# Kernel tuning notes

Measured on AMD Instinct MI355X. Metric: run time of the kernel, lower is better.

## Reference

```python
import jax, jax.numpy as jnp
import numpy as np

DIM = 64   # model dim == d_inner (expand=1)
Hh = 64
Ww = 64
BATCH = 4
D_IN = 64
N_ST = 8   # d_state
DT_R = 4   # dt_rank = ceil(dim/16)
K = 4      # depthwise conv kernel
NB = 8     # total CrossMambaBlocks: 4 (depth=1) + 4 final cross blocks


def setup_inputs():
    key = jax.random.key(0)
    ks = iter(jax.random.split(key, 40))
    def rn(shape, s=0.02):
        return jax.random.normal(next(ks), shape, jnp.float32) * s
    A_init = jnp.log(jnp.tile(jnp.arange(1, N_ST + 1, dtype=jnp.float32), (NB, D_IN, 1)))
    return dict(
        img1=rn((BATCH, DIM, Hh, Ww), 1.0), img2=rn((BATCH, DIM, Hh, Ww), 1.0),
        img1_sum=rn((BATCH, DIM, Hh, Ww), 1.0), img2_sum=rn((BATCH, DIM, Hh, Ww), 1.0),
        norm0_w=jnp.ones((NB, DIM)), norm0_b=jnp.zeros((NB, DIM)),
        norm1_w=jnp.ones((NB, DIM)), norm1_b=jnp.zeros((NB, DIM)),
        in_w=rn((NB, 2 * D_IN, DIM)), in_b=jnp.zeros((NB, 2 * D_IN)),
        conv_w_f=rn((NB, D_IN, 1, K), 0.1), conv_b_f=jnp.zeros((NB, D_IN)),
        conv_w_b=rn((NB, D_IN, 1, K), 0.1), conv_b_b=jnp.zeros((NB, D_IN)),
        xproj_w_f=rn((NB, DT_R + 2 * N_ST, D_IN)), xproj_w_b=rn((NB, DT_R + 2 * N_ST, D_IN)),
        dtproj_w_f=rn((NB, D_IN, DT_R), 0.1), dtproj_b_f=jnp.zeros((NB, D_IN)),
        dtproj_w_b=rn((NB, D_IN, DT_R), 0.1), dtproj_b_b=jnp.zeros((NB, D_IN)),
        A_log_f=A_init, A_log_b=A_init,
        D_f=jnp.ones((NB, D_IN)), D_b=jnp.ones((NB, D_IN)),
        ln_w=jnp.ones((NB, D_IN)), ln_b=jnp.zeros((NB, D_IN)),
        mout_w=rn((NB, DIM, D_IN)), mout_b=jnp.zeros((NB, DIM)),
        fop_w=rn((DIM, 2 * DIM)), fop_b=jnp.zeros((DIM,)),
    )


def _ln(x, w, b):
    m = x.mean(-1, keepdims=True)
    v = ((x - m) ** 2).mean(-1, keepdims=True)
    return (x - m) * jax.lax.rsqrt(v + 1e-5) * w + b


def _dwconv(x, w, b):
    # x: [b,L,d], w: [d,1,K] depthwise causal conv along L
    y = jax.lax.conv_general_dilated(
        x.transpose(0, 2, 1), w, (1,), [(K - 1, 0)],
        dimension_numbers=('NCH', 'OIH', 'NCH'),
        feature_group_count=x.shape[-1])
    return y.transpose(0, 2, 1) + b


def _ssm(u, dt, Bm, Cm, A, Dm):
    # u,dt: [b,L,d]; Bm,Cm: [b,L,n]; A: [d,n]; Dm: [d]
    dA = jnp.exp(dt[..., None] * A)                 # [b,L,d,n]
    dBu = (dt * u)[..., None] * Bm[:, :, None, :]   # [b,L,d,n]
    def step(h, xs):
        dA_t, dBu_t, C_t = xs
        h = dA_t * h + dBu_t
        return h, jnp.einsum('bdn,bn->bd', h, C_t)
    h0 = jnp.zeros(u.shape[:1] + A.shape, u.dtype)
    _, ys = jax.lax.scan(step, h0, (jnp.moveaxis(dA, 1, 0), jnp.moveaxis(dBu, 1, 0), jnp.moveaxis(Cm, 1, 0)))
    return jnp.moveaxis(ys, 0, 1) + u * Dm


def _direction(x_in, extra, conv_w, conv_b, xproj_w, dtproj_w, dtproj_b, A_log, Dm, flip):
    if flip:
        x_in = x_in[:, ::-1]
        extra = extra[:, ::-1]
    u = jax.nn.silu(_dwconv(x_in, conv_w, conv_b))
    dbl = jnp.einsum('bld,ed->ble', extra, xproj_w)     # cross: dt/B/C from extra embedding
    dtr = dbl[..., :DT_R]
    Bm = dbl[..., DT_R:DT_R + N_ST]
    Cm = dbl[..., DT_R + N_ST:]
    dt = jax.nn.softplus(jnp.einsum('blr,dr->bld', dtr, dtproj_w) + dtproj_b)
    y = _ssm(u, dt, Bm, Cm, -jnp.exp(A_log), Dm)
    if flip:
        y = y[:, ::-1]
    return y


def _cross_block(i, x, extra, p):
    skip = x
    x = _ln(x, p['norm0_w'][i], p['norm0_b'][i])
    extra = _ln(extra, p['norm1_w'][i], p['norm1_b'][i])
    xz = jnp.einsum('bld,ed->ble', x, p['in_w'][i]) + p['in_b'][i]
    x_in, z = xz[..., :D_IN], xz[..., D_IN:]
    y_f = _direction(x_in, extra, p['conv_w_f'][i], p['conv_b_f'][i], p['xproj_w_f'][i],
                     p['dtproj_w_f'][i], p['dtproj_b_f'][i], p['A_log_f'][i], p['D_f'][i], False)
    y_b = _direction(x_in, extra, p['conv_w_b'][i], p['conv_b_b'][i], p['xproj_w_b'][i],
                     p['dtproj_w_b'][i], p['dtproj_b_b'][i], p['A_log_b'][i], p['D_b'][i], True)
    y = 0.5 * (y_f + y_b)                    # if_devide_out=True
    y = _ln(y, p['ln_w'][i], p['ln_b'][i])   # use_norm=True
    y = y * jax.nn.silu(z)
    out = jnp.einsum('bld,ed->ble', y, p['mout_w'][i]) + p['mout_b'][i]
    return out + skip


def _forward(img1, img2, img1_sum, img2_sum, norm0_w, norm0_b, norm1_w, norm1_b, in_w, in_b,
             conv_w_f, conv_b_f, conv_w_b, conv_b_b, xproj_w_f, xproj_w_b,
             dtproj_w_f, dtproj_b_f, dtproj_w_b, dtproj_b_b, A_log_f, A_log_b,
             D_f, D_b, ln_w, ln_b, mout_w, mout_b, fop_w, fop_b):
    p = dict(norm0_w=norm0_w, norm0_b=norm0_b, norm1_w=norm1_w, norm1_b=norm1_b,
             in_w=in_w, in_b=in_b, conv_w_f=conv_w_f, conv_b_f=conv_b_f,
             conv_w_b=conv_w_b, conv_b_b=conv_b_b, xproj_w_f=xproj_w_f, xproj_w_b=xproj_w_b,
             dtproj_w_f=dtproj_w_f, dtproj_b_f=dtproj_b_f, dtproj_w_b=dtproj_w_b,
             dtproj_b_b=dtproj_b_b, A_log_f=A_log_f, A_log_b=A_log_b, D_f=D_f, D_b=D_b,
             ln_w=ln_w, ln_b=ln_b, mout_w=mout_w, mout_b=mout_b)
    def seq(t):
        b, c, h, w = t.shape
        return t.reshape(b, c, h * w).transpose(0, 2, 1)   # b (h w) c
    s1, s2, s1s, s2s = seq(img1), seq(img2), seq(img1_sum), seq(img2_sum)
    # depth=1 cross-fusion loop
    s1 = _cross_block(0, s1, s1s, p)
    s2 = _cross_block(1, s2, s2s, p)
    s1s = _cross_block(2, s1s, s1, p)
    s2s = _cross_block(3, s2s, s2, p)
    # final cross blocks
    i1l = _cross_block(4, s1, s2, p)
    i1g = _cross_block(5, s1, s2s, p)
    i2l = _cross_block(6, s2, s1, p)
    i2g = _cross_block(7, s2, s1s, p)
    c1 = jnp.concatenate([i1l, i1g], -1)
    c2 = jnp.concatenate([i2l, i2g], -1)
    fusion = jnp.einsum('ble,ce->blc', 0.5 * (c1 + c2), fop_w) + fop_b
    b = img1.shape[0]
    return fusion.transpose(0, 2, 1).reshape(b, DIM, Hh, Ww)


def reference(img1, img2, img1_sum, img2_sum, norm0_w, norm0_b, norm1_w, norm1_b, in_w, in_b,
              conv_w_f, conv_b_f, conv_w_b, conv_b_b, xproj_w_f, xproj_w_b,
              dtproj_w_f, dtproj_b_f, dtproj_w_b, dtproj_b_b, A_log_f, A_log_b,
              D_f, D_b, ln_w, ln_b, mout_w, mout_b, fop_w, fop_b):
    return _forward(img1, img2, img1_sum, img2_sum, norm0_w, norm0_b, norm1_w, norm1_b, in_w, in_b,
                    conv_w_f, conv_b_f, conv_w_b, conv_b_b, xproj_w_f, xproj_w_b,
                    dtproj_w_f, dtproj_b_f, dtproj_w_b, dtproj_b_b, A_log_f, A_log_b,
                    D_f, D_b, ln_w, ln_b, mout_w, mout_b, fop_w, fop_b)
```

## Files before the change

### kernel.cpp

```cpp
#include <hip/hip_runtime.h>
#include <hip/hip_bf16.h>

#define BX 4
#define LX 4096
#define DX 64
#define NX 8
#define TCH 16
#define NCH 256
#define BLD (BX*LX*DX)

typedef unsigned short u16;
typedef __attribute__((ext_vector_type(8))) short v8s;
typedef __attribute__((ext_vector_type(4))) float v4f;

#define L2E 1.44269504088896f
#define LN2 0.69314718055994531f

__device__ __forceinline__ float b2f(u16 u){ return __uint_as_float(((unsigned)u)<<16); }
__device__ __forceinline__ u16 f2b(float f){
  unsigned u = __float_as_uint(f);
  unsigned r = (u + 0x7FFFu + ((u>>16)&1u)) >> 16;
  return (u16)r;
}
__device__ __forceinline__ float siluf(float x){
  return x * __builtin_amdgcn_rcpf(1.f + __builtin_amdgcn_exp2f(-x*L2E));
}
__device__ __forceinline__ float softplusf(float x){
  const float t = __builtin_amdgcn_exp2f(-fabsf(x)*L2E);
  return fmaxf(x, 0.f) + LN2 * __builtin_amdgcn_logf(1.f + t);
}

__device__ __forceinline__ v4f mfma16(v8s a, v8s b, v4f c){
  return __builtin_amdgcn_mfma_f32_16x16x32_bf16(a, b, c, 0, 0, 0);
}
__device__ __forceinline__ void split8(const float* v, v8s& hi, v8s& lo){
  #pragma unroll
  for(int j=0;j<8;j++){
    const short h = (short)f2b(v[j]);
    hi[j] = h;
    lo[j] = (short)f2b(v[j] - b2f((u16)h));
  }
}
__device__ __forceinline__ void afrag(const float* tile, int lane, int k0, v8s& hi, v8s& lo){
  const float* p = tile + (lane&15)*72 + k0 + ((lane>>4)<<3);
  float v[8];
  const float4 a = *(const float4*)(p);
  const float4 b = *(const float4*)(p+4);
  v[0]=a.x; v[1]=a.y; v[2]=a.z; v[3]=a.w;
  v[4]=b.x; v[5]=b.y; v[6]=b.z; v[7]=b.w;
  split8(v, hi, lo);
}

struct Ctx {
  const float *nw0,*nb0,*nw1,*nb1;
  const float *inb;
  const float *convw,*convb;
  const float *dtw,*dtb;
  const float *A2,*Dp;
  const float *lnw,*lnb;
  const float *moutb;
  const float *fopb;
  const u16 *wih,*wil,*wxh,*wxl,*wmh,*wml,*wfh,*wfl;
  float *act[4], *outc[4];
  float *xin[4], *zz[4], *dbl[4], *Pp[4], *qq[4], *hin[4];
};

struct BlkDesc { int i; const float* x; const float* e; float* out; int slot; };
struct StageArgs { BlkDesc d[4]; };
struct SeqArgs { const void* src[4]; };

struct PrepEnt { const void* src; float* dst; int n; int mode; };
struct PrepAll { PrepEnt a[21]; };
struct WPrep { const void* sA; const void* sB; u16* dh; u16* dl; long off; int E; int KS; int kind; int i; };
struct WPrepAll { WPrep a[25]; };

__global__ __launch_bounds__(256) void k_prep(PrepAll pa, WPrepAll wa, SeqArgs sq, Ctx c, const u16* df){
  const bool isbf = (df[0] == 0x3F80u);
  __shared__ float ld[64*65];
  const int y = blockIdx.y;
  if(y < 21){
    PrepEnt p = pa.a[y];
    int idx = blockIdx.x*256 + threadIdx.x;
    if(idx < p.n){
      float v = isbf ? b2f(((const u16*)p.src)[idx]) : ((const float*)p.src)[idx];
      if(p.mode==2) v = -__expf(v) * L2E;
      p.dst[idx] = v;
    }
  } else if(y < 46){
    WPrep p = wa.a[y - 21];
    const int wv = threadIdx.x >> 6, lane = threadIdx.x & 63;
    const int idx = blockIdx.x*4 + wv;
    const int NT = (p.E + 15) >> 4;
    if(idx >= NT*p.KS) return;
    const int ct = idx / p.KS, ks = idx % p.KS;
    const int g  = ct*16 + (lane & 15);
    const int k0 = ks*32 + ((lane>>4)<<3);
    const int K  = p.KS*32;
    bool valid; long si = 0; const void* sp = p.sA;
    if(p.kind == 1){
      valid = (g < 40);
      const int dir = g/20, e = g - dir*20;
      if(dir) sp = p.sB;
      si = ((long)p.i*20 + e)*64 + k0;
    } else {
      valid = (g < p.E);
      si = p.off + (long)g*K + k0;
    }
    float v[8];
    #pragma unroll
    for(int j2=0;j2<8;j2++){
      float x = 0.f;
      if(valid) x = isbf ? b2f(((const u16*)sp)[si+j2]) : ((const float*)sp)[si+j2];
      v[j2] = x;
    }
    v8s hi, lo; split8(v, hi, lo);
    const size_t o = ((size_t)idx*64 + lane)*8;
    *(v8s*)(p.dh + o) = hi;
    *(v8s*)(p.dl + o) = lo;
  } else {
    const int sid = (y - 46)*16 + blockIdx.x;
    const int t4 = sid >> 8, b = (sid >> 6) & 3, l0 = (sid & 63)*64;
    float* dst = c.act[t4];
    const int tx = threadIdx.x & 63, ty = threadIdx.x >> 6;
    if(isbf){
      const u16* src = (const u16*)sq.src[t4];
      #pragma unroll
      for(int k=0;k<16;k++){ int d = k*4+ty; ld[d*65+tx] = b2f(src[(size_t)(b*64+d)*LX + l0+tx]); }
    } else {
      const float* src = (const float*)sq.src[t4];
      #pragma unroll
      for(int k=0;k<16;k++){ int d = k*4+ty; ld[d*65+tx] = src[(size_t)(b*64+d)*LX + l0+tx]; }
    }
    __syncthreads();
    #pragma unroll
    for(int k=0;k<16;k++){ int p = k*4+ty; dst[(size_t)(b*LX + l0+p)*64 + tx] = ld[tx*65+p]; }
  }
}

__device__ __forceinline__ void coop72(float* sb, const float* g, int t){
  #pragma unroll
  for(int k=0;k<4;k++){
    const int idx = k*256 + t;
    const int row = idx >> 4;
    const int c4  = (idx & 15) << 2;
    *(float4*)(sb + row*72 + c4) = *(const float4*)(g + (size_t)row*64 + c4);
  }
}
__device__ __forceinline__ void coop72_avg(float* sb, const float* g0, const float* g1, int t){
  #pragma unroll
  for(int k=0;k<4;k++){
    const int idx = k*256 + t;
    const int row = idx >> 4;
    const int c4  = (idx & 15) << 2;
    const float4 a = *(const float4*)(g0 + (size_t)row*64 + c4);
    const float4 b = *(const float4*)(g1 + (size_t)row*64 + c4);
    float4 o; o.x=0.5f*(a.x+b.x); o.y=0.5f*(a.y+b.y); o.z=0.5f*(a.z+b.z); o.w=0.5f*(a.w+b.w);
    *(float4*)(sb + row*72 + c4) = o;
  }
}
__device__ __forceinline__ void coop72_out(float* g, const float* sb, int t){
  #pragma unroll
  for(int k=0;k<4;k++){
    const int idx = k*256 + t;
    const int row = idx >> 4;
    const int c4  = (idx & 15) << 2;
    *(float4*)(g + (size_t)row*64 + c4) = *(const float4*)(sb + row*72 + c4);
  }
}

__device__ __forceinline__ void ln72(float* sb, int lane, const float* w, const float* b){
  float r[64];
  float* p = sb + lane*72;
  #pragma unroll
  for(int cc=0;cc<64;cc+=4){ float4 v = *(const float4*)(p+cc); r[cc]=v.x; r[cc+1]=v.y; r[cc+2]=v.z; r[cc+3]=v.w; }
  float m=0.f;
  #pragma unroll
  for(int d=0;d<64;d++) m += r[d];
  m *= (1.f/64.f);
  float va=0.f;
  #pragma unroll
  for(int d=0;d<64;d++){ float t=r[d]-m; va += t*t; }
  va *= (1.f/64.f);
  const float rs = rsqrtf(va + 1e-5f);
  #pragma unroll
  for(int d=0;d<64;d++) r[d] = (r[d]-m)*rs*w[d] + b[d];
  #pragma unroll
  for(int cc=0;cc<64;cc+=4){ float4 v={r[cc],r[cc+1],r[cc+2],r[cc+3]}; *(float4*)(p+cc)=v; }
}

__global__ __launch_bounds__(256) void k_front(Ctx c, StageArgs sa){
  __shared__ __align__(16) float sx[64*72];
  __shared__ __align__(16) float se[64*72];
  const BlkDesc bd = sa.d[blockIdx.y];
  const int i = bd.i;
  const int tile = blockIdx.x;
  const int b = tile >> 6;
  const int l0 = (tile & 63) << 6;
  const int bl0 = b*LX + l0;
  const int t = threadIdx.x;
  const int wave = t >> 6, lane = t & 63;

  coop72(sx, bd.x + (size_t)bl0*64, t);
  coop72(se, bd.e + (size_t)bl0*64, t);
  __syncthreads();
  if(wave == 0)      ln72(sx, lane, c.nw0 + i*64, c.nb0 + i*64);
  else if(wave == 1) ln72(se, lane, c.nw1 + i*64, c.nb1 + i*64);

  const v8s* WH = (const v8s*)c.wih + (size_t)i*1024;
  const v8s* WL = (const v8s*)c.wil + (size_t)i*1024;
  v8s cwh0 = WH[lane],     cwh1 = WH[64 + lane];
  v8s cwl0 = WL[lane],     cwl1 = WL[64 + lane];
  __syncthreads();

  const int m0 = wave*16;
  const int q  = lane >> 4;
  const int n15 = lane & 15;

  v8s xah[2], xal[2], eah[2], eal[2];
  afrag(sx + m0*72, lane, 0,  xah[0], xal[0]);
  afrag(sx + m0*72, lane, 32, xah[1], xal[1]);
  afrag(se + m0*72, lane, 0,  eah[0], eal[0]);
  afrag(se + m0*72, lane, 32, eah[1], eal[1]);
  __syncthreads();

  {
    #pragma unroll 1
    for(int ct=0; ct<8; ct++){
      v8s nwh0, nwh1, nwl0, nwl1;
      if(ct < 7){
        nwh0 = WH[((ct+1)*2+0)*64 + lane]; nwh1 = WH[((ct+1)*2+1)*64 + lane];
        nwl0 = WL[((ct+1)*2+0)*64 + lane]; nwl1 = WL[((ct+1)*2+1)*64 + lane];
      }
      const int colg = ct*16 + n15;
      const float bias = c.inb[i*128 + colg];
      v4f acc = {bias, bias, bias, bias};
      acc = mfma16(xah[0], cwl0, acc);
      acc = mfma16(xal[0], cwh0, acc);
      acc = mfma16(xah[0], cwh0, acc);
      acc = mfma16(xah[1], cwl1, acc);
      acc = mfma16(xal[1], cwh1, acc);
      acc = mfma16(xah[1], cwh1, acc);
      float* so = (colg < 64) ? sx : se;
      const int col = colg & 63;
      #pragma unroll
      for(int r=0;r<4;r++) so[(m0 + q*4 + r)*72 + col] = acc[r];
      cwh0 = nwh0; cwh1 = nwh1; cwl0 = nwl0; cwl1 = nwl1;
    }
  }
  {
    const v8s* XH = (const v8s*)c.wxh + (size_t)i*384;
    const v8s* XL = (const v8s*)c.wxl + (size_t)i*384;
    #pragma unroll
    for(int ct=0; ct<3; ct++){
      v4f acc = {0.f,0.f,0.f,0.f};
      #pragma unroll
      for(int ks=0; ks<2; ks++){
        const v8s wh = XH[(ct*2+ks)*64 + lane];
        const v8s wl = XL[(ct*2+ks)*64 + lane];
        acc = mfma16(eah[ks], wl, acc);
        acc = mfma16(eal[ks], wh, acc);
        acc = mfma16(eah[ks], wh, acc);
      }
      const int g = ct*16 + n15;
      if(g < 40){
        const int dir = (g >= 20);
        const int e = g - dir*20;
        float* dp = c.dbl[bd.slot] + (size_t)dir*((size_t)BX*LX*20);
        #pragma unroll
        for(int r=0;r<4;r++){
          const int row = m0 + q*4 + r;
          dp[(size_t)(bl0+row)*20 + e] = acc[r];
        }
      }
    }
  }
  __syncthreads();
  coop72_out(c.xin[bd.slot] + (size_t)bl0*64, sx, t);
  coop72_out(c.zz[bd.slot]  + (size_t)bl0*64, se, t);
}

template<int DIR>
__device__ __forceinline__ void scan1_dir(const float* xs, const float* meta,
    const float4 cwv, const float cbv, const float4 dwv, const float dtbv,
    const float* A2, float* h, float& S){
  #pragma unroll
  for(int t=0;t<TCH;t++){
    float w0,w1,w2,xc; int lr;
    if(DIR==0){ lr=t;       w0=xs[t];    w1=xs[t+1];  w2=xs[t+2];  xc=xs[t+3]; }
    else      { lr=15-t;    w0=xs[18-t]; w1=xs[17-t]; w2=xs[16-t]; xc=xs[15-t]; }
    const float u = siluf(cwv.x*w0 + cwv.y*w1 + cwv.z*w2 + cwv.w*xc + cbv);
    const float* m = meta + lr*20;
    const float4 m0 = *(const float4*)(m);
    const float dt = softplusf(m0.x*dwv.x + m0.y*dwv.y + m0.z*dwv.z + m0.w*dwv.w + dtbv);
    const float du = dt*u;
    const float4 mb0 = *(const float4*)(m+4);
    const float4 mb1 = *(const float4*)(m+8);
    const float Bv[8] = {mb0.x,mb0.y,mb0.z,mb0.w,mb1.x,mb1.y,mb1.z,mb1.w};
    #pragma unroll
    for(int n=0;n<8;n++){
      const float dA = __builtin_amdgcn_exp2f(dt*A2[n]);
      h[n] = dA*h[n] + du*Bv[n];
    }
    S += dt;
  }
}

__global__ __launch_bounds__(64) void k_scan1(Ctx c, StageArgs sa){
  __shared__ __align__(16) float meta[TCH*20];
  const int zid = blockIdx.z;
  const int j = zid >> 1, dir = zid & 1;
  const BlkDesc bd = sa.d[j];
  const int i = bd.i, slot = bd.slot;
  const int ch = blockIdx.x, b = blockIdx.y;
  const int d = threadIdx.x;
  const int pb = (dir*8 + i)*64 + d;

  const float4 cwv = *(const float4*)(c.convw + (size_t)pb*4);
  const float  cbv = c.convb[pb];
  const float4 dwv = *(const float4*)(c.dtw + (size_t)pb*4);
  const float  dtbv = c.dtb[pb];
  const float4 A2a = *(const float4*)(c.A2 + (size_t)pb*8);
  const float4 A2b = *(const float4*)(c.A2 + (size_t)pb*8 + 4);
  float A2[8] = {A2a.x,A2a.y,A2a.z,A2a.w,A2b.x,A2b.y,A2b.z,A2b.w};

  {
    const float4* s = (const float4*)(c.dbl[slot] + (size_t)dir*((size_t)BX*LX*20)
                                      + (size_t)(b*LX + ch*TCH)*20);
    float4* dst = (float4*)meta;
    #pragma unroll
    for(int k=0;k<2;k++){ int idx = k*64 + d; if(idx < 80) dst[idx] = s[idx]; }
  }
  __syncthreads();

  const int base = ch*TCH;
  const float* X = c.xin[slot] + (size_t)b*LX*64 + d;
  float xs[19];
  if(dir==0){
    #pragma unroll
    for(int k=0;k<19;k++){ const int r = base - 3 + k; xs[k] = (r>=0) ? X[(size_t)r*64] : 0.f; }
  } else {
    #pragma unroll
    for(int k=0;k<19;k++){ const int r = base + k; xs[k] = (r<LX) ? X[(size_t)r*64] : 0.f; }
  }

  float h[8];
  #pragma unroll
  for(int n=0;n<8;n++) h[n]=0.f;
  float S = 0.f;
  if(dir==0) scan1_dir<0>(xs, meta, cwv, cbv, dwv, dtbv, A2, h, S);
  else       scan1_dir<1>(xs, meta, cwv, cbv, dwv, dtbv, A2, h, S);

  float* Pw = c.Pp[slot] + (size_t)(dir*NCH + ch)*((size_t)BX*512) + (size_t)b*512 + d;
  float* Qw = c.qq[slot] + (size_t)(dir*NCH + ch)*((size_t)BX*512) + (size_t)b*512 + d;
  #pragma unroll
  for(int n=0;n<8;n++){
    Pw[n*64] = __builtin_amdgcn_exp2f(A2[n]*S);
    Qw[n*64] = h[n];
  }
}

__global__ __launch_bounds__(64) void k_mid(Ctx c, StageArgs sa){
  const int b = blockIdx.x >> 3;
  const int seg = blockIdx.x & 7;
  const int dir = blockIdx.y & 1, j = blockIdx.y >> 1;
  const BlkDesc bd = sa.d[j];
  const int slot = bd.slot;
  const int nd = seg*64 + threadIdx.x;
  const size_t base = (size_t)dir*NCH*((size_t)BX*512) + (size_t)b*512 + nd;
  const size_t STR = (size_t)BX*512;
  const float* P = c.Pp[slot] + base;
  const float* Q = c.qq[slot] + base;
  float* H = c.hin[slot] + base;
  float h = 0.f;
  float Pv[32], Qv[32];
  #pragma unroll 1
  for(int g=0; g<NCH/32; g++){
    #pragma unroll
    for(int k=0;k<32;k++){
      const int ch = dir ? (NCH-1 - (g*32+k)) : (g*32+k);
      Pv[k] = P[(size_t)ch*STR]; Qv[k] = Q[(size_t)ch*STR];
    }
    #pragma unroll
    for(int k=0;k<32;k++){
      const int ch = dir ? (NCH-1 - (g*32+k)) : (g*32+k);
      H[(size_t)ch*STR] = h;
      h = fmaf(Pv[k], h, Qv[k]);
    }
  }
}

__global__ __launch_bounds__(256) void k_back(Ctx c, StageArgs sa){
  __shared__ __align__(16) float sy[64*72];
  __shared__ __align__(16) float smeta[64*40];
  const BlkDesc bd = sa.d[blockIdx.y];
  const int i = bd.i, slot = bd.slot;
  const int tile = blockIdx.x;
  const int b = tile >> 6;
  const int l0 = (tile & 63) << 6;
  const int bl0 = b*LX + l0;
  const int t = threadIdx.x;
  const int wave = t >> 6, lane = t & 63;

  #pragma unroll
  for(int d2=0; d2<2; d2++){
    const float4* s = (const float4*)(c.dbl[slot] + (size_t)d2*((size_t)BX*LX*20) + (size_t)bl0*20);
    #pragma unroll
    for(int k=0;k<2;k++){
      const int idx = k*256 + t;
      if(idx < 320){
        const int row = idx/5, e4 = idx - row*5;
        *(float4*)(smeta + row*40 + d2*20 + e4*4) = s[idx];
      }
    }
  }
  __syncthreads();

  const int m0 = wave*16;
  {
    const int ch = (tile & 63)*4 + wave;
    const int d2 = lane;
    const float* X = c.xin[slot] + (size_t)b*LX*64 + d2;
    float xs[22];
    #pragma unroll
    for(int k=0;k<22;k++){
      const int r = l0 + m0 + k - 3;
      xs[k] = (r>=0 && r<LX) ? X[(size_t)r*64] : 0.f;
    }
    #pragma unroll
    for(int dir=0; dir<2; dir++){
      const int pb = (dir*8 + i)*64 + d2;
      const float4 cwv = *(const float4*)(c.convw + (size_t)pb*4);
      const float  cbv = c.convb[pb];
      const float4 dwv = *(const float4*)(c.dtw + (size_t)pb*4);
      const float  dtbv = c.dtb[pb];
      const float4 A2a = *(const float4*)(c.A2 + (size_t)pb*8);
      const float4 A2b = *(const float4*)(c.A2 + (size_t)pb*8 + 4);
      const float A2r[8] = {A2a.x,A2a.y,A2a.z,A2a.w,A2b.x,A2b.y,A2b.z,A2b.w};
      const float Dv = c.Dp[pb];
      float h[8];
      const float* hp = c.hin[slot] + (size_t)(dir*NCH + ch)*((size_t)BX*512) + (size_t)b*512 + d2;
      #pragma unroll
      for(int n=0;n<8;n++) h[n] = hp[n*64];
      #pragma unroll
      for(int k=0;k<16;k++){
        const int lr = dir ? (m0+15-k) : (m0+k);
        const float w0 = dir ? xs[21-k] : xs[k];
        const float w1 = dir ? xs[20-k] : xs[k+1];
        const float w2 = dir ? xs[19-k] : xs[k+2];
        const float xc = dir ? xs[18-k] : xs[k+3];
        const float u = siluf(cwv.x*w0 + cwv.y*w1 + cwv.z*w2 + cwv.w*xc + cbv);
        const float* m = smeta + lr*40 + dir*20;
        const float4 m0v = *(const float4*)(m);
        const float dt = softplusf(m0v.x*dwv.x + m0v.y*dwv.y + m0v.z*dwv.z + m0v.w*dwv.w + dtbv);
        const float du = dt*u;
        const float4 mb0 = *(const float4*)(m+4);
        const float4 mb1 = *(const float4*)(m+8);
        const float Bv[8] = {mb0.x,mb0.y,mb0.z,mb0.w,mb1.x,mb1.y,mb1.z,mb1.w};
        float yv = u*Dv;
        #pragma unroll
        for(int n=0;n<8;n++){
          const float dA = __builtin_amdgcn_exp2f(dt*A2r[n]);
          h[n] = dA*h[n] + du*Bv[n];
        }
        const float4 mc0 = *(const float4*)(m+12);
        const float4 mc1 = *(const float4*)(m+16);
        const float Cv[8] = {mc0.x,mc0.y,mc0.z,mc0.w,mc1.x,mc1.y,mc1.z,mc1.w};
        #pragma unroll
        for(int n=0;n<8;n++) yv += h[n]*Cv[n];
        if(dir==0) sy[lr*72 + d2] = 0.5f*yv;
        else       sy[lr*72 + d2] += 0.5f*yv;
      }
    }
  }
  __syncthreads();
  if(wave == 0){
    ln72(sy, lane, c.lnw + i*64, c.lnb + i*64);
    float* p = sy + lane*72;
    const float4* zp = (const float4*)(c.zz[slot] + (size_t)(bl0+lane)*64);
    #pragma unroll
    for(int d3=0;d3<16;d3++){
      const float4 z4 = zp[d3];
      p[d3*4+0] *= siluf(z4.x); p[d3*4+1] *= siluf(z4.y);
      p[d3*4+2] *= siluf(z4.z); p[d3*4+3] *= siluf(z4.w);
    }
  }
  __syncthreads();

  const int q  = lane >> 4;
  const int n15 = lane & 15;
  v8s ah[2], al[2];
  afrag(sy + m0*72, lane, 0,  ah[0], al[0]);
  afrag(sy + m0*72, lane, 32, ah[1], al[1]);
  __syncthreads();

  const v8s* WH = (const v8s*)c.wmh + (size_t)i*512;
  const v8s* WL = (const v8s*)c.wml + (size_t)i*512;
  #pragma unroll
  for(int ct=0; ct<4; ct++){
    const int col = ct*16 + n15;
    const float bias = c.moutb[i*64 + col];
    v4f acc = {bias, bias, bias, bias};
    #pragma unroll
    for(int ks=0; ks<2; ks++){
      const v8s wh = WH[(ct*2+ks)*64 + lane];
      const v8s wl = WL[(ct*2+ks)*64 + lane];
      acc = mfma16(ah[ks], wl, acc);
      acc = mfma16(al[ks], wh, acc);
      acc = mfma16(ah[ks], wh, acc);
    }
    #pragma unroll
    for(int r=0;r<4;r++) sy[(m0 + q*4 + r)*72 + col] = acc[r];
  }
  __syncthreads();
  #pragma unroll
  for(int k=0;k<4;k++){
    const int idx = k*256 + t;
    const int row = idx >> 4;
    const int c4  = (idx & 15) << 2;
    const float4 sk = *(const float4*)(bd.x + (size_t)(bl0+row)*64 + c4);
    const float4 a  = *(const float4*)(sy + row*72 + c4);
    float4 o; o.x=a.x+sk.x; o.y=a.y+sk.y; o.z=a.z+sk.z; o.w=a.w+sk.w;
    *(float4*)(bd.out + (size_t)(bl0+row)*64 + c4) = o;
  }
}

__global__ __launch_bounds__(256) void k_fusion(Ctx c, void* outp, const u16* df){
  const bool isbf = (df[0] == 0x3F80u);
  __shared__ __align__(16) float sL[64*72];
  __shared__ __align__(16) float sH[64*72];
  __shared__ __align__(16) float sT[64*68];
  const int tile = blockIdx.x;
  const int b = tile >> 6;
  const int l0 = (tile & 63) << 6;
  const int bl0 = b*LX + l0;
  const int t = threadIdx.x;
  const int wave = t >> 6, lane = t & 63;

  coop72_avg(sL, c.outc[0] + (size_t)bl0*64, c.outc[2] + (size_t)bl0*64, t);
  coop72_avg(sH, c.outc[1] + (size_t)bl0*64, c.outc[3] + (size_t)bl0*64, t);
  __syncthreads();

  const int m0 = wave*16;
  const int q  = lane >> 4;
  const int n15 = lane & 15;
  v8s ah[4], al[4];
  afrag(sL + m0*72, lane, 0,  ah[0], al[0]);
  afrag(sL + m0*72, lane, 32, ah[1], al[1]);
  afrag(sH + m0*72, lane, 0,  ah[2], al[2]);
  afrag(sH + m0*72, lane, 32, ah[3], al[3]);
  const v8s* WH = (const v8s*)c.wfh;
  const v8s* WL = (const v8s*)c.wfl;
  #pragma unroll 2
  for(int ct=0; ct<4; ct++){
    const int col = ct*16 + n15;
    const float bias = c.fopb[col];
    v4f acc = {bias, bias, bias, bias};
    #pragma unroll
    for(int ks=0; ks<4; ks++){
      const v8s wh = WH[(ct*4+ks)*64 + lane];
      const v8s wl = WL[(ct*4+ks)*64 + lane];
      acc = mfma16(ah[ks], wl, acc);
      acc = mfma16(al[ks], wh, acc);
      acc = mfma16(ah[ks], wh, acc);
    }
    #pragma unroll
    for(int r=0;r<4;r++) sT[col*68 + m0 + q*4 + r] = acc[r];
  }
  __syncthreads();

  const int o  = t >> 2;
  const int p0 = (t & 3) * 16;
  float v[16];
  #pragma unroll
  for(int k=0;k<16;k+=4){
    const float4 x = *(const float4*)(sT + o*68 + p0 + k);
    v[k]=x.x; v[k+1]=x.y; v[k+2]=x.z; v[k+3]=x.w;
  }
  const size_t off = (size_t)(b*64+o)*LX + l0 + p0;
  if(isbf){
    u16 hb[16];
    #pragma unroll
    for(int k=0;k<16;k++) hb[k] = f2b(v[k]);
    uint4 u0, u1;
    u0.x = hb[0] | ((unsigned)hb[1]<<16);  u0.y = hb[2] | ((unsigned)hb[3]<<16);
    u0.z = hb[4] | ((unsigned)hb[5]<<16);  u0.w = hb[6] | ((unsigned)hb[7]<<16);
    u1.x = hb[8] | ((unsigned)hb[9]<<16);  u1.y = hb[10]| ((unsigned)hb[11]<<16);
    u1.z = hb[12]| ((unsigned)hb[13]<<16); u1.w = hb[14]| ((unsigned)hb[15]<<16);
    *(uint4*)((u16*)outp + off)     = u0;
    *(uint4*)((u16*)outp + off + 8) = u1;
  } else {
    float* fo = (float*)outp + off;
    #pragma unroll
    for(int k=0;k<16;k+=4){ float4 x={v[k],v[k+1],v[k+2],v[k+3]}; *(float4*)(fo+k)=x; }
  }
}

extern "C" void kernel_launch(void* const* d_in, const int* in_sizes, int n_in,
                              void* d_out, int out_size, void* d_ws, size_t ws_size,
                              hipStream_t stream){
  (void)in_sizes; (void)out_size;
  if(n_in < 30) return;
  const u16* df = (const u16*)d_in[22];
  float* w = (float*)d_ws;
  size_t off = 0;
  auto al = [&](size_t n){ float* p = w + off; off += n; return p; };

  Ctx c;
  float* nw0 = al(512);  float* nb0 = al(512);
  float* nw1 = al(512);  float* nb1 = al(512);
  float* inb = al(1024);
  float* convw = al(4096); float* convb = al(1024);
  float* dtw = al(4096); float* dtb = al(1024);
  float* A2 = al(8192);  float* Dp = al(1024);
  float* lnw = al(512);  float* lnb = al(512);
  float* moutb = al(512);
  float* fopb = al(64);
  c.nw0=nw0; c.nb0=nb0; c.nw1=nw1; c.nb1=nb1;
  c.inb=inb; c.convw=convw; c.convb=convb;
  c.dtw=dtw; c.dtb=dtb; c.A2=A2; c.Dp=Dp;
  c.lnw=lnw; c.lnb=lnb; c.moutb=moutb; c.fopb=fopb;

  u16* wih = (u16*)al(32768); u16* wil = (u16*)al(32768);
  u16* wxh = (u16*)al(12288); u16* wxl = (u16*)al(12288);
  u16* wmh = (u16*)al(16384); u16* wml = (u16*)al(16384);
  u16* wfh = (u16*)al(4096);  u16* wfl = (u16*)al(4096);
  c.wih=wih; c.wil=wil; c.wxh=wxh; c.wxl=wxl; c.wmh=wmh; c.wml=wml; c.wfh=wfh; c.wfl=wfl;

  for(int k=0;k<4;k++) c.act[k]  = al(BLD);
  for(int k=0;k<4;k++) c.outc[k] = al(BLD);

  const size_t CHW = 2*(size_t)NCH*BX*512;
  const size_t SLOT = (size_t)BLD + BLD + 2*(size_t)BX*LX*20 + 3*CHW;
  const size_t avail = ws_size/4;
  int nslots = 4;
  while(nslots>1 && off + (size_t)nslots*SLOT > avail) nslots >>= 1;
  for(int s=0;s<nslots;s++){
    c.xin[s]=al(BLD); c.zz[s]=al(BLD); c.dbl[s]=al(2*(size_t)BX*LX*20);
    c.Pp[s]=al(CHW); c.qq[s]=al(CHW); c.hin[s]=al(CHW);
  }
  for(int s=nslots;s<4;s++){
    c.xin[s]=c.xin[0]; c.zz[s]=c.zz[0]; c.dbl[s]=c.dbl[0];
    c.Pp[s]=c.Pp[0]; c.qq[s]=c.qq[0]; c.hin[s]=c.hin[0];
  }

  PrepAll pa;
  int kk = 0;
  auto add = [&](int idx, float* dst, int n, int mode){
    pa.a[kk].src=d_in[idx]; pa.a[kk].dst=dst; pa.a[kk].n=n; pa.a[kk].mode=mode; kk++;
  };
  add(4,  nw0, 512, 0); add(5,  nb0, 512, 0);
  add(6,  nw1, 512, 0); add(7,  nb1, 512, 0);
  add(9,  inb, 1024, 0);
  add(10, convw, 2048, 0);      add(11, convb, 512, 0);
  add(12, convw+2048, 2048, 0); add(13, convb+512, 512, 0);
  add(16, dtw, 2048, 0);        add(17, dtb, 512, 0);
  add(18, dtw+2048, 2048, 0);   add(19, dtb+512, 512, 0);
  add(20, A2, 4096, 2);         add(21, A2+4096, 4096, 2);
  add(22, Dp, 512, 0);          add(23, Dp+512, 512, 0);
  add(24, lnw, 512, 0);         add(25, lnb, 512, 0);
  add(27, moutb, 512, 0);
  add(29, fopb, 64, 0);

  WPrepAll wa;
  for(int i=0;i<8;i++) wa.a[i]    = { d_in[8],  nullptr,  wih+(size_t)i*8192, wil+(size_t)i*8192, (long)i*8192, 128, 2, 0, i };
  for(int i=0;i<8;i++) wa.a[8+i]  = { d_in[14], d_in[15], wxh+(size_t)i*3072, wxl+(size_t)i*3072, 0,            48, 2, 1, i };
  for(int i=0;i<8;i++) wa.a[16+i] = { d_in[26], nullptr,  wmh+(size_t)i*4096, wml+(size_t)i*4096, (long)i*4096, 64, 2, 0, i };
  wa.a[24] = { d_in[28], nullptr, wfh, wfl, 0, 64, 4, 0, 0 };

  SeqArgs sq;
  for(int t=0;t<4;t++) sq.src[t] = d_in[t];

  k_prep<<<dim3(16,110),256,0,stream>>>(pa, wa, sq, c, df);

  BlkDesc R1[2] = {{0, c.act[0], c.act[2], c.act[0], 0},
                   {1, c.act[1], c.act[3], c.act[1], 0}};
  BlkDesc R2[4] = {{2, c.act[2], c.act[0], c.act[2], 0},
                   {3, c.act[3], c.act[1], c.act[3], 0},
                   {4, c.act[0], c.act[1], c.outc[0], 0},
                   {6, c.act[1], c.act[0], c.outc[2], 0}};
  BlkDesc R3[2] = {{5, c.act[0], c.act[3], c.outc[1], 0},
                   {7, c.act[1], c.act[2], c.outc[3], 0}};

  auto run = [&](BlkDesc* ds, int cnt){
    for(int k=0;k<cnt;k+=nslots){
      int n = cnt-k; if(n>nslots) n = nslots;
      StageArgs sa;
      for(int j=0;j<n;j++){ sa.d[j] = ds[k+j]; sa.d[j].slot = j; }
      for(int j=n;j<4;j++) sa.d[j] = sa.d[0];
      k_front<<<dim3(256,n),      256, 0, stream>>>(c, sa);
      k_scan1<<<dim3(NCH,BX,2*n),  64, 0, stream>>>(c, sa);
      k_mid  <<<dim3(BX*8,2*n),    64, 0, stream>>>(c, sa);
      k_back <<<dim3(256,n),      256, 0, stream>>>(c, sa);
    }
  };
  run(R1,2); run(R2,4); run(R3,2);
  k_fusion<<<256,256,0,stream>>>(c, d_out, df);
}
```

Baseline: 345.7 us.

## Split front projection across two blocks and run both scan directions concurrently in back

k_front is launched with a z dimension of 2. One half computes the x-projection plus the x_proj/dt outputs, the other computes the z-projection, and each preloads all of its weights into registers. k_back goes from 256 to 512 threads, so the forward and backward scan directions run in separate waves with separate shared buffers, summed afterward, and the out-projection columns are split between the two groups. This doubles parallelism per tile to hide latency, at the cost of redundant input loads and layernorm work in k_front, more shared memory, and higher register pressure.

After: 347.6 us. No clear change (+0.6%).

```diff
diff --git a/kernel.cpp b/kernel.cpp
--- a/kernel.cpp
+++ b/kernel.cpp
@@ -194,60 +194,48 @@
   const BlkDesc bd = sa.d[blockIdx.y];
   const int i = bd.i;
   const int tile = blockIdx.x;
+  const int half = blockIdx.z;
   const int b = tile >> 6;
   const int l0 = (tile & 63) << 6;
   const int bl0 = b*LX + l0;
   const int t = threadIdx.x;
   const int wave = t >> 6, lane = t & 63;
-
-  coop72(sx, bd.x + (size_t)bl0*64, t);
-  coop72(se, bd.e + (size_t)bl0*64, t);
-  __syncthreads();
-  if(wave == 0)      ln72(sx, lane, c.nw0 + i*64, c.nb0 + i*64);
-  else if(wave == 1) ln72(se, lane, c.nw1 + i*64, c.nb1 + i*64);
-
-  const v8s* WH = (const v8s*)c.wih + (size_t)i*1024;
-  const v8s* WL = (const v8s*)c.wil + (size_t)i*1024;
-  v8s cwh0 = WH[lane],     cwh1 = WH[64 + lane];
-  v8s cwl0 = WL[lane],     cwl1 = WL[64 + lane];
-  __syncthreads();
-
   const int m0 = wave*16;
   const int q  = lane >> 4;
   const int n15 = lane & 15;
-
-  v8s xah[2], xal[2], eah[2], eal[2];
-  afrag(sx + m0*72, lane, 0,  xah[0], xal[0]);
-  afrag(sx + m0*72, lane, 32, xah[1], xal[1]);
-  afrag(se + m0*72, lane, 0,  eah[0], eal[0]);
-  afrag(se + m0*72, lane, 32, eah[1], eal[1]);
-  __syncthreads();
-
-  {
-    #pragma unroll 1
-    for(int ct=0; ct<8; ct++){
-      v8s nwh0, nwh1, nwl0, nwl1;
-      if(ct < 7){
-        nwh0 = WH[((ct+1)*2+0)*64 + lane]; nwh1 = WH[((ct+1)*2+1)*64 + lane];
-        nwl0 = WL[((ct+1)*2+0)*64 + lane]; nwl1 = WL[((ct+1)*2+1)*64 + lane];
-      }
+  const v8s* WH = (const v8s*)c.wih + (size_t)i*1024;
+  const v8s* WL = (const v8s*)c.wil + (size_t)i*1024;
+
+  if(half == 0){
+    coop72(sx, bd.x + (size_t)bl0*64, t);
+    coop72(se, bd.e + (size_t)bl0*64, t);
+    __syncthreads();
+    if(wave == 0)      ln72(sx, lane, c.nw0 + i*64, c.nb0 + i*64);
+    else if(wave == 1) ln72(se, lane, c.nw1 + i*64, c.nb1 + i*64);
+    v8s wh[8], wl[8];
+    #pragma unroll
+    for(int k=0;k<8;k++){ wh[k] = WH[k*64 + lane]; wl[k] = WL[k*64 + lane]; }
+    __syncthreads();
+    v8s xah[2], xal[2], eah[2], eal[2];
+    afrag(sx + m0*72, lane, 0,  xah[0], xal[0]);
+    afrag(sx + m0*72, lane, 32, xah[1], xal[1]);
+    afrag(se + m0*72, lane, 0,  eah[0], eal[0]);
+    afrag(se + m0*72, lane, 32, eah[1], eal[1]);
+    __syncthreads();
+    #pragma unroll
+    for(int ct=0; ct<4; ct++){
       const int colg = ct*16 + n15;
       const float bias = c.inb[i*128 + colg];
       v4f acc = {bias, bias, bias, bias};
-      acc = mfma16(xah[0], cwl0, acc);
-      acc = mfma16(xal[0], cwh0, acc);
-      acc = mfma16(xah[0], cwh0, acc);
-      acc = mfma16(xah[1], cwl1, acc);
-      acc = mfma16(xal[1], cwh1, acc);
-      acc = mfma16(xah[1], cwh1, acc);
-      float* so = (colg < 64) ? sx : se;
-      const int col = colg & 63;
-      #pragma unroll
-      for(int r=0;r<4;r++) so[(m0 + q*4 + r)*72 + col] = acc[r];
-      cwh0 = nwh0; cwh1 = nwh1; cwl0 = nwl0; cwl1 = nwl1;
-    }
-  }
-  {
+      acc = mfma16(xah[0], wl[ct*2+0], acc);
+      acc = mfma16(xal[0], wh[ct*2+0], acc);
+      acc = mfma16(xah[0], wh[ct*2+0], acc);
+      acc = mfma16(xah[1], wl[ct*2+1], acc);
+      acc = mfma16(xal[1], wh[ct*2+1], acc);
+      acc = mfma16(xah[1], wh[ct*2+1], acc);
+      #pragma unroll
+      for(int r=0;r<4;r++) sx[(m0 + q*4 + r)*72 + colg] = acc[r];
+    }
     const v8s* XH = (const v8s*)c.wxh + (size_t)i*384;
     const v8s* XL = (const v8s*)c.wxl + (size_t)i*384;
     #pragma unroll
@@ -255,11 +243,11 @@
       v4f acc = {0.f,0.f,0.f,0.f};
       #pragma unroll
       for(int ks=0; ks<2; ks++){
-        const v8s wh = XH[(ct*2+ks)*64 + lane];
-        const v8s wl = XL[(ct*2+ks)*64 + lane];
-        acc = mfma16(eah[ks], wl, acc);
-        acc = mfma16(eal[ks], wh, acc);
-        acc = mfma16(eah[ks], wh, acc);
+        const v8s xwh = XH[(ct*2+ks)*64 + lane];
+        const v8s xwl = XL[(ct*2+ks)*64 + lane];
+        acc = mfma16(eah[ks], xwl, acc);
+        acc = mfma16(eal[ks], xwh, acc);
+        acc = mfma16(eah[ks], xwh, acc);
       }
       const int g = ct*16 + n15;
       if(g < 40){
@@ -273,10 +261,37 @@
         }
       }
     }
-  }
-  __syncthreads();
-  coop72_out(c.xin[bd.slot] + (size_t)bl0*64, sx, t);
-  coop72_out(c.zz[bd.slot]  + (size_t)bl0*64, se, t);
+    __syncthreads();
+    coop72_out(c.xin[bd.slot] + (size_t)bl0*64, sx, t);
+  } else {
+    coop72(sx, bd.x + (size_t)bl0*64, t);
+    __syncthreads();
+    if(wave == 0) ln72(sx, lane, c.nw0 + i*64, c.nb0 + i*64);
+    v8s wh[8], wl[8];
+    #pragma unroll
+    for(int k=0;k<8;k++){ wh[k] = WH[(8+k)*64 + lane]; wl[k] = WL[(8+k)*64 + lane]; }
+    __syncthreads();
+    v8s xah[2], xal[2];
+    afrag(sx + m0*72, lane, 0,  xah[0], xal[0]);
+    afrag(sx + m0*72, lane, 32, xah[1], xal[1]);
+    #pragma unroll
+    for(int ct=0; ct<4; ct++){
+      const int colg = (ct+4)*16 + n15;
+      const float bias = c.inb[i*128 + colg];
+      v4f acc = {bias, bias, bias, bias};
+      acc = mfma16(xah[0], wl[ct*2+0], acc);
+      acc = mfma16(xal[0], wh[ct*2+0], acc);
+      acc = mfma16(xah[0], wh[ct*2+0], acc);
+      acc = mfma16(xah[1], wl[ct*2+1], acc);
+      acc = mfma16(xal[1], wh[ct*2+1], acc);
+      acc = mfma16(xah[1], wh[ct*2+1], acc);
+      const int col = colg - 64;
+      #pragma unroll
+      for(int r=0;r<4;r++) se[(m0 + q*4 + r)*72 + col] = acc[r];
+    }
+    __syncthreads();
+    coop72_out(c.zz[bd.slot] + (size_t)bl0*64, se, t);
+  }
 }
 
 template<int DIR>
@@ -389,8 +404,9 @@
   }
 }
 
-__global__ __launch_bounds__(256) void k_back(Ctx c, StageArgs sa){
-  __shared__ __align__(16) float sy[64*72];
+__global__ __launch_bounds__(512) void k_back(Ctx c, StageArgs sa){
+  __shared__ __align__(16) float sy0[64*72];
+  __shared__ __align__(16) float sy1[64*72];
   __shared__ __align__(16) float smeta[64*40];
   const BlkDesc bd = sa.d[blockIdx.y];
   const int i = bd.i, slot = bd.slot;
@@ -400,82 +416,95 @@
   const int bl0 = b*LX + l0;
   const int t = threadIdx.x;
   const int wave = t >> 6, lane = t & 63;
-
-  #pragma unroll
-  for(int d2=0; d2<2; d2++){
-    const float4* s = (const float4*)(c.dbl[slot] + (size_t)d2*((size_t)BX*LX*20) + (size_t)bl0*20);
-    #pragma unroll
-    for(int k=0;k<2;k++){
-      const int idx = k*256 + t;
-      if(idx < 320){
-        const int row = idx/5, e4 = idx - row*5;
-        *(float4*)(smeta + row*40 + d2*20 + e4*4) = s[idx];
-      }
+  const int wq = wave & 3, dir = wave >> 2;
+  const int m0 = wq*16;
+  const int q  = lane >> 4;
+  const int n15 = lane & 15;
+
+  #pragma unroll
+  for(int k=0;k<2;k++){
+    const int idx = k*512 + t;
+    if(idx < 640){
+      const int d2 = (idx >= 320);
+      const int r  = idx - (d2 ? 320 : 0);
+      const int row = r/5, e4 = r - row*5;
+      const float4* s = (const float4*)(c.dbl[slot] + (size_t)d2*((size_t)BX*LX*20) + (size_t)bl0*20);
+      *(float4*)(smeta + row*40 + d2*20 + e4*4) = s[r];
     }
   }
   __syncthreads();
 
-  const int m0 = wave*16;
   {
-    const int ch = (tile & 63)*4 + wave;
+    const int ch = (tile & 63)*4 + wq;
     const int d2 = lane;
     const float* X = c.xin[slot] + (size_t)b*LX*64 + d2;
-    float xs[22];
-    #pragma unroll
-    for(int k=0;k<22;k++){
-      const int r = l0 + m0 + k - 3;
-      xs[k] = (r>=0 && r<LX) ? X[(size_t)r*64] : 0.f;
-    }
-    #pragma unroll
-    for(int dir=0; dir<2; dir++){
-      const int pb = (dir*8 + i)*64 + d2;
-      const float4 cwv = *(const float4*)(c.convw + (size_t)pb*4);
-      const float  cbv = c.convb[pb];
-      const float4 dwv = *(const float4*)(c.dtw + (size_t)pb*4);
-      const float  dtbv = c.dtb[pb];
-      const float4 A2a = *(const float4*)(c.A2 + (size_t)pb*8);
-      const float4 A2b = *(const float4*)(c.A2 + (size_t)pb*8 + 4);
-      const float A2r[8] = {A2a.x,A2a.y,A2a.z,A2a.w,A2b.x,A2b.y,A2b.z,A2b.w};
-      const float Dv = c.Dp[pb];
-      float h[8];
-      const float* hp = c.hin[slot] + (size_t)(dir*NCH + ch)*((size_t)BX*512) + (size_t)b*512 + d2;
-      #pragma unroll
-      for(int n=0;n<8;n++) h[n] = hp[n*64];
-      #pragma unroll
-      for(int k=0;k<16;k++){
-        const int lr = dir ? (m0+15-k) : (m0+k);
-        const float w0 = dir ? xs[21-k] : xs[k];
-        const float w1 = dir ? xs[20-k] : xs[k+1];
-        const float w2 = dir ? xs[19-k] : xs[k+2];
-        const float xc = dir ? xs[18-k] : xs[k+3];
-        const float u = siluf(cwv.x*w0 + cwv.y*w1 + cwv.z*w2 + cwv.w*xc + cbv);
-        const float* m = smeta + lr*40 + dir*20;
-        const float4 m0v = *(const float4*)(m);
-        const float dt = softplusf(m0v.x*dwv.x + m0v.y*dwv.y + m0v.z*dwv.z + m0v.w*dwv.w + dtbv);
-        const float du = dt*u;
-        const float4 mb0 = *(const float4*)(m+4);
-        const float4 mb1 = *(const float4*)(m+8);
-        const float Bv[8] = {mb0.x,mb0.y,mb0.z,mb0.w,mb1.x,mb1.y,mb1.z,mb1.w};
-        float yv = u*Dv;
-        #pragma unroll
-        for(int n=0;n<8;n++){
-          const float dA = __builtin_amdgcn_exp2f(dt*A2r[n]);
-          h[n] = dA*h[n] + du*Bv[n];
-        }
-        const float4 mc0 = *(const float4*)(m+12);
-        const float4 mc1 = *(const float4*)(m+16);
-        const float Cv[8] = {mc0.x,mc0.y,mc0.z,mc0.w,mc1.x,mc1.y,mc1.z,mc1.w};
-        #pragma unroll
-        for(int n=0;n<8;n++) yv += h[n]*Cv[n];
-        if(dir==0) sy[lr*72 + d2] = 0.5f*yv;
-        else       sy[lr*72 + d2] += 0.5f*yv;
+    const int base = l0 + m0;
+    float xs[19];
+    if(dir==0){
+      #pragma unroll
+      for(int k=0;k<19;k++){ const int r = base - 3 + k; xs[k] = (r>=0) ? X[(size_t)r*64] : 0.f; }
+    } else {
+      #pragma unroll
+      for(int k=0;k<19;k++){ const int r = base + k; xs[k] = (r<LX) ? X[(size_t)r*64] : 0.f; }
+    }
+    const int pb = (dir*8 + i)*64 + d2;
+    const float4 cwv = *(const float4*)(c.convw + (size_t)pb*4);
+    const float  cbv = c.convb[pb];
+    const float4 dwv = *(const float4*)(c.dtw + (size_t)pb*4);
+    const float  dtbv = c.dtb[pb];
+    const float4 A2a = *(const float4*)(c.A2 + (size_t)pb*8);
+    const float4 A2b = *(const float4*)(c.A2 + (size_t)pb*8 + 4);
+    const float A2r[8] = {A2a.x,A2a.y,A2a.z,A2a.w,A2b.x,A2b.y,A2b.z,A2b.w};
+    const float Dv = c.Dp[pb];
+    float h[8];
+    const float* hp = c.hin[slot] + (size_t)(dir*NCH + ch)*((size_t)BX*512) + (size_t)b*512 + d2;
+    #pragma unroll
+    for(int n=0;n<8;n++) h[n] = hp[n*64];
+    float* syD = dir ? sy1 : sy0;
+    #pragma unroll
+    for(int k=0;k<16;k++){
+      const int lr = dir ? (m0+15-k) : (m0+k);
+      const float w0 = dir ? xs[18-k] : xs[k];
+      const float w1 = dir ? xs[17-k] : xs[k+1];
+      const float w2 = dir ? xs[16-k] : xs[k+2];
+      const float xc = dir ? xs[15-k] : xs[k+3];
+      const float u = siluf(cwv.x*w0 + cwv.y*w1 + cwv.z*w2 + cwv.w*xc + cbv);
+      const float* m = smeta + lr*40 + dir*20;
+      const float4 m0v = *(const float4*)(m);
+      const float dt = softplusf(m0v.x*dwv.x + m0v.y*dwv.y + m0v.z*dwv.z + m0v.w*dwv.w + dtbv);
+      const float du = dt*u;
+      const float4 mb0 = *(const float4*)(m+4);
+      const float4 mb1 = *(const float4*)(m+8);
+      const float Bv[8] = {mb0.x,mb0.y,mb0.z,mb0.w,mb1.x,mb1.y,mb1.z,mb1.w};
+      float yv = u*Dv;
+      #pragma unroll
+      for(int n=0;n<8;n++){
+        const float dA = __builtin_amdgcn_exp2f(dt*A2r[n]);
+        h[n] = dA*h[n] + du*Bv[n];
       }
-    }
+      const float4 mc0 = *(const float4*)(m+12);
+      const float4 mc1 = *(const float4*)(m+16);
+      const float Cv[8] = {mc0.x,mc0.y,mc0.z,mc0.w,mc1.x,mc1.y,mc1.z,mc1.w};
+      #pragma unroll
+      for(int n=0;n<8;n++) yv += h[n]*Cv[n];
+      syD[lr*72 + d2] = 0.5f*yv;
+    }
+  }
+  __syncthreads();
+  #pragma unroll
+  for(int k=0;k<2;k++){
+    const int idx = k*512 + t;
+    const int row = idx >> 4;
+    const int c4  = (idx & 15) << 2;
+    float4 a = *(const float4*)(sy0 + row*72 + c4);
+    const float4 bb = *(const float4*)(sy1 + row*72 + c4);
+    a.x += bb.x; a.y += bb.y; a.z += bb.z; a.w += bb.w;
+    *(float4*)(sy0 + row*72 + c4) = a;
   }
   __syncthreads();
   if(wave == 0){
-    ln72(sy, lane, c.lnw + i*64, c.lnb + i*64);
-    float* p = sy + lane*72;
+    ln72(sy0, lane, c.lnw + i*64, c.lnb + i*64);
+    float* p = sy0 + lane*72;
     const float4* zp = (const float4*)(c.zz[slot] + (size_t)(bl0+lane)*64);
     #pragma unroll
     for(int d3=0;d3<16;d3++){
@@ -486,17 +515,14 @@
   }
   __syncthreads();
 
-  const int q  = lane >> 4;
-  const int n15 = lane & 15;
   v8s ah[2], al[2];
-  afrag(sy + m0*72, lane, 0,  ah[0], al[0]);
-  afrag(sy + m0*72, lane, 32, ah[1], al[1]);
-  __syncthreads();
-
+  afrag(sy0 + m0*72, lane, 0,  ah[0], al[0]);
+  afrag(sy0 + m0*72, lane, 32, ah[1], al[1]);
   const v8s* WH = (const v8s*)c.wmh + (size_t)i*512;
   const v8s* WL = (const v8s*)c.wml + (size_t)i*512;
   #pragma unroll
-  for(int ct=0; ct<4; ct++){
+  for(int j2=0; j2<2; j2++){
+    const int ct = dir*2 + j2;
     const int col = ct*16 + n15;
     const float bias = c.moutb[i*64 + col];
     v4f acc = {bias, bias, bias, bias};
@@ -509,16 +535,16 @@
       acc = mfma16(ah[ks], wh, acc);
     }
     #pragma unroll
-    for(int r=0;r<4;r++) sy[(m0 + q*4 + r)*72 + col] = acc[r];
+    for(int r=0;r<4;r++) sy1[(m0 + q*4 + r)*72 + col] = acc[r];
   }
   __syncthreads();
   #pragma unroll
-  for(int k=0;k<4;k++){
-    const int idx = k*256 + t;
+  for(int k=0;k<2;k++){
+    const int idx = k*512 + t;
     const int row = idx >> 4;
     const int c4  = (idx & 15) << 2;
     const float4 sk = *(const float4*)(bd.x + (size_t)(bl0+row)*64 + c4);
-    const float4 a  = *(const float4*)(sy + row*72 + c4);
+    const float4 a  = *(const float4*)(sy1 + row*72 + c4);
     float4 o; o.x=a.x+sk.x; o.y=a.y+sk.y; o.z=a.z+sk.z; o.w=a.w+sk.w;
     *(float4*)(bd.out + (size_t)(bl0+row)*64 + c4) = o;
   }
@@ -687,10 +713,10 @@
       StageArgs sa;
       for(int j=0;j<n;j++){ sa.d[j] = ds[k+j]; sa.d[j].slot = j; }
       for(int j=n;j<4;j++) sa.d[j] = sa.d[0];
-      k_front<<<dim3(256,n),      256, 0, stream>>>(c, sa);
+      k_front<<<dim3(256,n,2),    256, 0, stream>>>(c, sa);
       k_scan1<<<dim3(NCH,BX,2*n),  64, 0, stream>>>(c, sa);
       k_mid  <<<dim3(BX*8,2*n),    64, 0, stream>>>(c, sa);
-      k_back <<<dim3(256,n),      256, 0, stream>>>(c, sa);
+      k_back <<<dim3(256,n),      512, 0, stream>>>(c, sa);
     }
   };
   run(R1,2); run(R2,4); run(R3,2);
```
